# Optimization experiments

Measured on AMD Instinct MI355X. Metric: run time of the kernel, lower is better.

Reference implementation:

```python
import jax, jax.numpy as jnp
import numpy as np

N_NODES = 100000
TYPE_COUNTS = [40000, 40000, 20000]
RAW_DIMS = [512, 256, 128]
D = 64          # node_feature_dim
H = 8           # num_attention_heads
M = 2           # num_metapaths
E = 500000      # edges per metapath
SEM = 128       # semantic_attention_dim
NUM_CLS = 8
T = 40000       # num target nodes
SLOPE = 0.01    # leaky relu slope


def setup_inputs() -> dict:
    key = jax.random.key(0)
    ks = jax.random.split(key, 16)
    inp = {}
    inp['target_nodes'] = jax.random.randint(ks[0], (T,), 0, N_NODES)
    inp['metapath_0'] = jax.random.randint(ks[1], (E, 2), 0, N_NODES)
    inp['metapath_1'] = jax.random.randint(ks[2], (E, 2), 0, N_NODES)
    # contiguous blocks per node type (type t occupies a contiguous index range)
    inp['node_type_mapping'] = jnp.concatenate(
        [jnp.full((c,), t, dtype=jnp.int32) for t, c in enumerate(TYPE_COUNTS)])
    for t, (c, r) in enumerate(zip(TYPE_COUNTS, RAW_DIMS)):
        inp[f'node_feat_{t}'] = jax.random.normal(ks[3 + t], (c, r), dtype=jnp.float32)
        xav = float(np.sqrt(2.0) * np.sqrt(2.0 / (D + r)))
        inp[f'W{t}'] = jax.random.normal(ks[6 + t], (D, r), dtype=jnp.float32) * xav
        inp[f'b{t}'] = jnp.zeros((D,), dtype=jnp.float32)
    inp['node_attention'] = jax.random.normal(ks[9], (M, H, 2 * D), dtype=jnp.float32) * 0.05
    inp['Wsem'] = jax.random.normal(ks[10], (SEM, H * D), dtype=jnp.float32) * 0.05
    inp['bsem'] = jnp.zeros((SEM,), dtype=jnp.float32)
    inp['a_sem'] = jax.random.normal(ks[11], (SEM,), dtype=jnp.float32) * 0.05
    inp['Wcls'] = jax.random.normal(ks[12], (NUM_CLS, H * D), dtype=jnp.float32) * 0.05
    inp['bcls'] = jnp.zeros((NUM_CLS,), dtype=jnp.float32)
    return inp


def _metapath_agg(node_features, mp, attn_vec, target_nodes, n_nodes):
    # mp: [E, 2] (col 0 = neighbor/src, col -1 = current/dst); attn_vec: [H, 2D]
    src = mp[:, 0]
    dst = mp[:, -1]
    h_src = node_features[src]                        # [E, D] gather
    h_dst = node_features[dst]                        # [E, D] gather
    e = jnp.concatenate([h_dst, h_src], axis=-1)      # [E, 2D]
    score = e @ attn_vec.T                            # [E, H]
    score = jnp.where(score > 0, score, SLOPE * score)  # LeakyReLU
    # edge softmax over incoming edges of each destination node (per head)
    m = jax.ops.segment_max(score, dst, num_segments=n_nodes)
    ex = jnp.exp(score - m[dst])
    den = jax.ops.segment_sum(ex, dst, num_segments=n_nodes)
    attn = ex / den[dst]                              # [E, H]
    weighted = h_src[:, None, :] * attn[:, :, None]   # [E, H, D]
    agg = jax.ops.segment_sum(weighted, dst, num_segments=n_nodes)  # [N, H, D]
    return agg[target_nodes]                          # [T, H, D]


def reference(target_nodes, metapath_0, metapath_1, node_type_mapping,
              node_feat_0, node_feat_1, node_feat_2,
              W0, b0, W1, b1, W2, b2,
              node_attention, Wsem, bsem, a_sem, Wcls, bcls):
    n_nodes = node_type_mapping.shape[0]
    # node types are contiguous index blocks, so per-type projection + concat
    # reproduces the original scatter-by-type exactly (dropout rate is 0)
    node_features = jnp.concatenate([
        node_feat_0 @ W0.T + b0,
        node_feat_1 @ W1.T + b1,
        node_feat_2 @ W2.T + b2,
    ], axis=0)                                        # [N, D]
    h_list = [
        _metapath_agg(node_features, metapath_0, node_attention[0], target_nodes, n_nodes),
        _metapath_agg(node_features, metapath_1, node_attention[1], target_nodes, n_nodes),
    ]
    h = jnp.stack(h_list).reshape(M, -1, H * D)       # [M, T, H*D]
    s = jnp.tanh(jnp.einsum('mtd,sd->mts', h, Wsem) + bsem)  # [M, T, SEM]
    scores = jnp.mean(s @ a_sem, axis=1)              # [M] semantic attention
    beta = jax.nn.softmax(scores)                     # [M]
    embeddings = jnp.einsum('m,mtd->td', beta, h)     # [T, H*D]
    cls_logits = embeddings @ Wcls.T + bcls           # [T, NUM_CLS]
    return cls_logits, embeddings
```

## Files before the change

kernel.cpp:

```cpp
#include <hip/hip_runtime.h>
#include <hip/hip_bf16.h>

#define N_NODES 100000
#define EDGES   500000
#define T_TGT   40000
#define NH      8
#define NSEM    128
#define NCLS    8
#define SLOPE   0.01f
#define NCHUNK  25
#define PPAD    36

#define AS1 __attribute__((address_space(1)))
#define AS3 __attribute__((address_space(3)))

typedef __attribute__((ext_vector_type(8))) __bf16 bf16x8;
typedef __attribute__((ext_vector_type(4))) float f32x4;

__global__ __launch_bounds__(256) void proj_mfma(
        const float* __restrict__ A0, const float* __restrict__ W0,
        const float* __restrict__ b0,
        const float* __restrict__ A1, const float* __restrict__ W1,
        const float* __restrict__ b1,
        const float* __restrict__ A2, const float* __restrict__ W2,
        const float* __restrict__ b2,
        float* __restrict__ out) {
    __shared__ __bf16 Ah[2][128 * PPAD], Al[2][128 * PPAD];
    __shared__ __bf16 Wh[2][64 * PPAD],  Wl[2][64 * PPAD];
    int bx = blockIdx.x;
    const float *A, *W, *bias; int M, K, r0; float* op;
    if (bx < 313)      { A = A0; W = W0; bias = b0; M = 40000; K = 512;
                         r0 = bx * 128;         op = out; }
    else if (bx < 626) { A = A1; W = W1; bias = b1; M = 40000; K = 256;
                         r0 = (bx - 313) * 128; op = out + (size_t)40000 * 64; }
    else               { A = A2; W = W2; bias = b2; M = 20000; K = 128;
                         r0 = (bx - 626) * 128; op = out + (size_t)80000 * 64; }
    int tid = threadIdx.x;
    int wave = tid >> 6, lane = tid & 63;
    int arow = tid >> 1;
    int acol = (tid & 1) * 16;
    int wrow = tid & 63;
    int wcol = wave * 8;
    const float* Arp = A + (size_t)(r0 + arow) * K + acol;
    const float* Wrp = W + (size_t)wrow * K + wcol;
    bool aval = (r0 + arow) < M;

    float4 av0, av1, av2, av3, wv0, wv1;
    auto gload = [&](int k0) {
        float4 z = make_float4(0.f, 0.f, 0.f, 0.f);
        av0 = aval ? *(const float4*)(Arp + k0 + 0)  : z;
        av1 = aval ? *(const float4*)(Arp + k0 + 4)  : z;
        av2 = aval ? *(const float4*)(Arp + k0 + 8)  : z;
        av3 = aval ? *(const float4*)(Arp + k0 + 12) : z;
        wv0 = *(const float4*)(Wrp + k0 + 0);
        wv1 = *(const float4*)(Wrp + k0 + 4);
    };
    auto cvt_write = [&](int buf) {
        float xa[16] = {av0.x, av0.y, av0.z, av0.w, av1.x, av1.y, av1.z, av1.w,
                        av2.x, av2.y, av2.z, av2.w, av3.x, av3.y, av3.z, av3.w};
        bf16x8 ah2[2], al2[2];
        #pragma unroll
        for (int j = 0; j < 16; j++) {
            __bf16 h = (__bf16)xa[j];
            ah2[j >> 3][j & 7] = h;
            al2[j >> 3][j & 7] = (__bf16)(xa[j] - (float)h);
        }
        *(bf16x8*)&Ah[buf][arow * PPAD + acol]     = ah2[0];
        *(bf16x8*)&Ah[buf][arow * PPAD + acol + 8] = ah2[1];
        *(bf16x8*)&Al[buf][arow * PPAD + acol]     = al2[0];
        *(bf16x8*)&Al[buf][arow * PPAD + acol + 8] = al2[1];
        float xw[8] = {wv0.x, wv0.y, wv0.z, wv0.w, wv1.x, wv1.y, wv1.z, wv1.w};
        bf16x8 wh2, wl2;
        #pragma unroll
        for (int j = 0; j < 8; j++) {
            __bf16 h = (__bf16)xw[j];
            wh2[j] = h;
            wl2[j] = (__bf16)(xw[j] - (float)h);
        }
        *(bf16x8*)&Wh[buf][wrow * PPAD + wcol] = wh2;
        *(bf16x8*)&Wl[buf][wrow * PPAD + wcol] = wl2;
    };

    int mrow = lane & 15, koff = (lane >> 4) * 8;
    f32x4 acc[2][4] = {};
    int nsteps = K >> 5;

    gload(0);
    cvt_write(0);
    __syncthreads();
    for (int t = 0; t < nsteps; t++) {
        int cur = t & 1;
        if (t + 1 < nsteps) gload((t + 1) * 32);
        __builtin_amdgcn_sched_barrier(0);
        bf16x8 afh[2], afl[2], bfh[4], bfl[4];
        #pragma unroll
        for (int mi = 0; mi < 2; mi++) {
            int r = wave * 32 + mi * 16 + mrow;
            afh[mi] = *(const bf16x8*)&Ah[cur][r * PPAD + koff];
            afl[mi] = *(const bf16x8*)&Al[cur][r * PPAD + koff];
        }
        #pragma unroll
        for (int ni = 0; ni < 4; ni++) {
            int r = ni * 16 + mrow;
            bfh[ni] = *(const bf16x8*)&Wh[cur][r * PPAD + koff];
            bfl[ni] = *(const bf16x8*)&Wl[cur][r * PPAD + koff];
        }
        #pragma unroll
        for (int mi = 0; mi < 2; mi++)
            #pragma unroll
            for (int ni = 0; ni < 4; ni++) {
                acc[mi][ni] = __builtin_amdgcn_mfma_f32_16x16x32_bf16(afh[mi], bfh[ni], acc[mi][ni], 0, 0, 0);
                acc[mi][ni] = __builtin_amdgcn_mfma_f32_16x16x32_bf16(afh[mi], bfl[ni], acc[mi][ni], 0, 0, 0);
                acc[mi][ni] = __builtin_amdgcn_mfma_f32_16x16x32_bf16(afl[mi], bfh[ni], acc[mi][ni], 0, 0, 0);
            }
        if (t + 1 < nsteps) cvt_write(cur ^ 1);
        __syncthreads();
    }
    #pragma unroll
    for (int ni = 0; ni < 4; ni++) {
        int col = ni * 16 + mrow;
        float bv = bias[col];
        #pragma unroll
        for (int mi = 0; mi < 2; mi++) {
            int row = r0 + wave * 32 + mi * 16 + (lane >> 4) * 4;
            #pragma unroll
            for (int j = 0; j < 4; j++)
                if (row + j < M)
                    op[(size_t)(row + j) * 64 + col] = acc[mi][ni][j] + bv;
        }
    }
}

__global__ __launch_bounds__(256) void attn_proj(const float* __restrict__ nf,
        const float* __restrict__ na, float* __restrict__ proj) {
    __shared__ float ft[64][65];
    __shared__ float at[32][65];
    int tid = threadIdx.x;
    int n0 = blockIdx.x * 64;
    #pragma unroll
    for (int i = 0; i < 8; i++) {
        int lin = tid + i * 256;
        int j = lin >> 6, d = lin & 63;
        int m = j >> 4, side = (j >> 3) & 1, h = j & 7;
        at[j][d] = na[m * 1024 + h * 128 + side * 64 + d];
    }
    #pragma unroll
    for (int i = 0; i < 4; i++) {
        int lin = tid + i * 256;
        int row = lin >> 4;
        int c4 = (lin & 15) * 4;
        int gn = n0 + row;
        float4 v = make_float4(0.f, 0.f, 0.f, 0.f);
        if (gn < N_NODES) v = *(const float4*)(nf + (size_t)gn * 64 + c4);
        ft[row][c4 + 0] = v.x; ft[row][c4 + 1] = v.y;
        ft[row][c4 + 2] = v.z; ft[row][c4 + 3] = v.w;
    }
    __syncthreads();
    int node = tid >> 2;
    int jg = tid & 3;
    float acc[8] = {};
    for (int d = 0; d < 64; d++) {
        float f = ft[node][d];
        #pragma unroll
        for (int jj = 0; jj < 8; jj++)
            acc[jj] = fmaf(f, at[jg * 8 + jj][d], acc[jj]);
    }
    int gn = n0 + node;
    if (gn < N_NODES) {
        float4 o0 = make_float4(acc[0], acc[1], acc[2], acc[3]);
        float4 o1 = make_float4(acc[4], acc[5], acc[6], acc[7]);
        *(float4*)(proj + (size_t)gn * 32 + jg * 8) = o0;
        *(float4*)(proj + (size_t)gn * 32 + jg * 8 + 4) = o1;
    }
}

__global__ void hist_targets(const int* __restrict__ tgt, int* __restrict__ tcnt) {
    int i = blockIdx.x * 256 + threadIdx.x;
    if (i < T_TGT) atomicAdd(&tcnt[tgt[i]], 1);
}

__global__ void hist_edges(const int* __restrict__ mp, const int* __restrict__ tcnt,
                           int* __restrict__ ecnt) {
    int e = blockIdx.x * 256 + threadIdx.x;
    if (e < EDGES) {
        int dst = mp[2 * e + 1];
        if (tcnt[dst] > 0) atomicAdd(&ecnt[dst], 1);
    }
}

__global__ __launch_bounds__(1024) void scan_partial(const int* __restrict__ counts,
        int* __restrict__ partials) {
    int a = blockIdx.y, bx = blockIdx.x;
    const int* in = counts + (size_t)a * N_NODES;
    int base = bx * 4096 + threadIdx.x * 4;
    int s = 0;
    #pragma unroll
    for (int i = 0; i < 4; i++) {
        int idx = base + i;
        if (idx < N_NODES) s += in[idx];
    }
    #pragma unroll
    for (int off = 32; off; off >>= 1) s += __shfl_xor(s, off);
    __shared__ int red[16];
    int lane = threadIdx.x & 63, w = threadIdx.x >> 6;
    if (lane == 0) red[w] = s;
    __syncthreads();
    if (threadIdx.x < 16) {
        int x = red[threadIdx.x];
        #pragma unroll
        for (int off = 8; off; off >>= 1) x += __shfl_xor(x, off);
        if (threadIdx.x == 0) partials[a * 32 + bx] = x;
    }
}

__global__ void scan_partials(const int* __restrict__ partials,
        int* __restrict__ choff, int* __restrict__ offs) {
    int w = threadIdx.x >> 6, lane = threadIdx.x & 63;
    if (w < 3 && lane < 32) {
        int v = (lane < NCHUNK) ? partials[w * 32 + lane] : 0;
        int x = v;
        #pragma unroll
        for (int off = 1; off < 32; off <<= 1) {
            int y = __shfl_up(x, off);
            if (lane >= off) x += y;
        }
        if (lane < NCHUNK) choff[w * 32 + lane] = x - v;
        if (lane == NCHUNK - 1) offs[(size_t)w * (N_NODES + 1) + N_NODES] = x;
    }
}

__global__ __launch_bounds__(1024) void scan_final(const int* __restrict__ counts,
        const int* __restrict__ choff, int* __restrict__ offs, int* __restrict__ curs) {
    int a = blockIdx.y, bx = blockIdx.x;
    const int* in = counts + (size_t)a * N_NODES;
    int* out = offs + (size_t)a * (N_NODES + 1);
    int* cur = curs + (size_t)a * N_NODES;
    int tid = threadIdx.x, lane = tid & 63, w = tid >> 6;
    int base = bx * 4096 + tid * 4;
    int v[4], sum4 = 0;
    #pragma unroll
    for (int i = 0; i < 4; i++) {
        int idx = base + i;
        v[i] = (idx < N_NODES) ? in[idx] : 0;
        sum4 += v[i];
    }
    int x = sum4;
    #pragma unroll
    for (int off = 1; off < 64; off <<= 1) {
        int y = __shfl_up(x, off);
        if (lane >= off) x += y;
    }
    __shared__ int wred[16], wexc[16];
    if (lane == 63) wred[w] = x;
    __syncthreads();
    if (tid < 16) {
        int s = wred[tid], xs = s;
        #pragma unroll
        for (int off = 1; off < 16; off <<= 1) {
            int y = __shfl_up(xs, off);
            if (tid >= off) xs += y;
        }
        wexc[tid] = xs - s;
    }
    __syncthreads();
    int off0 = choff[a * 32 + bx] + wexc[w] + (x - sum4);
    int run = 0;
    #pragma unroll
    for (int i = 0; i < 4; i++) {
        int idx = base + i;
        if (idx < N_NODES) { out[idx] = off0 + run; cur[idx] = off0 + run; }
        run += v[i];
    }
}

__global__ void scatter_targets(const int* __restrict__ tgt, int* __restrict__ tcur,
                                int* __restrict__ tlist) {
    int i = blockIdx.x * 256 + threadIdx.x;
    if (i < T_TGT) {
        int n = tgt[i];
        int p = atomicAdd(&tcur[n], 1);
        tlist[p] = i;
    }
}

__global__ __launch_bounds__(256) void scatter_score(const int* __restrict__ mp,
        const int* __restrict__ tcnt, int* __restrict__ ecur,
        int* __restrict__ elist, __bf16* __restrict__ exs,
        const float* __restrict__ proj, int m) {
    int e = blockIdx.x * 256 + threadIdx.x;
    if (e >= EDGES) return;
    int src = mp[2 * e], dst = mp[2 * e + 1];
    if (tcnt[dst] <= 0) return;
    int p = atomicAdd(&ecur[dst], 1);
    elist[p] = src;
    const float* adp = proj + (size_t)dst * 32 + m * 16;
    const float* asp = proj + (size_t)src * 32 + m * 16 + 8;
    float4 ad0 = *(const float4*)(adp), ad1 = *(const float4*)(adp + 4);
    float4 as0 = *(const float4*)(asp), as1 = *(const float4*)(asp + 4);
    float ads[8] = {ad0.x, ad0.y, ad0.z, ad0.w, ad1.x, ad1.y, ad1.z, ad1.w};
    float ass[8] = {as0.x, as0.y, as0.z, as0.w, as1.x, as1.y, as1.z, as1.w};
    bf16x8 exv;
    #pragma unroll
    for (int h = 0; h < 8; h++) {
        float sc = ads[h] + ass[h];
        sc = sc > 0.f ? sc : SLOPE * sc;
        exv[h] = (__bf16)__expf(sc);
    }
    *(bf16x8*)(exs + (size_t)p * 8) = exv;
}

__global__ void build_ulist(const int* __restrict__ tcnt, int* __restrict__ ulist,
                            int* __restrict__ ucount) {
    int n = blockIdx.x * 256 + threadIdx.x;
    if (n < N_NODES && tcnt[n] > 0) {
        int u = atomicAdd(ucount, 1);
        ulist[u] = n;
    }
}

__global__ void cvt_bf16(const float* __restrict__ in, __bf16* __restrict__ out, int n) {
    int i = blockIdx.x * 256 + threadIdx.x;
    if (i < n) out[i] = (__bf16)in[i];
}

__global__ __launch_bounds__(256) void agg_kernel(
        const int* __restrict__ ulist, const int* __restrict__ ctrl_i,
        const int* __restrict__ offs,
        const int* __restrict__ esrc,
        const __bf16* __restrict__ exs,
        const float* __restrict__ nf,
        const int* __restrict__ tlist,
        __bf16* hb0, __bf16* hb1) {
    int m = blockIdx.y;
    int wslot = blockIdx.x * 4 + (threadIdx.x >> 6);
    int lane = threadIdx.x & 63;
    int ucount = ctrl_i[0];
    if (wslot >= ucount) return;
    int node = __builtin_amdgcn_readfirstlane(ulist[wslot]);
    const int* eo = offs + (size_t)m * (N_NODES + 1);
    int e0 = eo[node], e1 = eo[node + 1];
    const int* srcs = esrc + (size_t)m * EDGES;
    const __bf16* exm = exs + (size_t)m * EDGES * 8;
    float acc[8] = {};
    float dacc[8] = {};
    for (int e = e0; e < e1; e++) {
        int s = srcs[e];
        bf16x8 pb = *(const bf16x8*)(exm + (size_t)e * 8);
        float v = nf[(size_t)s * 64 + lane];
        #pragma unroll
        for (int h = 0; h < 8; h++) {
            float pw = (float)pb[h];
            dacc[h] += pw;
            acc[h] = fmaf(pw, v, acc[h]);
        }
    }
    #pragma unroll
    for (int h = 0; h < 8; h++)
        acc[h] *= (dacc[h] > 0.f) ? 1.0f / dacc[h] : 0.f;
    const int* to = offs + (size_t)2 * (N_NODES + 1);
    int t0 = to[node], t1 = to[node + 1];
    __bf16* hb = (m == 0) ? hb0 : hb1;
    for (int ti = t0; ti < t1; ti++) {
        int t = tlist[ti];
        __bf16* dst = hb + (size_t)t * 512;
        #pragma unroll
        for (int h = 0; h < 8; h++) dst[h * 64 + lane] = (__bf16)acc[h];
    }
}

__global__ __launch_bounds__(256) void sem_mfma(
        const __bf16* __restrict__ hb,
        const __bf16* __restrict__ Wb,
        const float* __restrict__ bsem, const float* __restrict__ a_sem,
        float* __restrict__ scores) {
    __shared__ __bf16 As[2][64 * 64];
    __shared__ __bf16 Bs[2][128 * 64];
    int m = blockIdx.y;
    int tid = threadIdx.x;
    int wave = tid >> 6, lane = tid & 63;
    const __bf16* A0 = hb + (size_t)m * T_TGT * 512 + (size_t)blockIdx.x * 64 * 512;

    int srow = lane >> 3;
    int scol = (lane & 7) * 8;

    auto stage = [&](int buf, int k0) {
        #pragma unroll
        for (int j = 0; j < 2; j++) {
            int row = j * 32 + wave * 8 + srow;
            const __bf16* gp = A0 + (size_t)row * 512 + k0 + scol;
            __bf16* lp = &As[buf][(j * 32 + wave * 8) * 64];
            __builtin_amdgcn_global_load_lds((const AS1 void*)gp,
                                             (AS3 void*)lp, 16, 0, 0);
        }
        #pragma unroll
        for (int j = 0; j < 4; j++) {
            int row = j * 32 + wave * 8 + srow;
            const __bf16* gp = Wb + (size_t)row * 512 + k0 + scol;
            __bf16* lp = &Bs[buf][(j * 32 + wave * 8) * 64];
            __builtin_amdgcn_global_load_lds((const AS1 void*)gp,
                                             (AS3 void*)lp, 16, 0, 0);
        }
    };

    int mrow = lane & 15;
    int kq = lane >> 4;
    f32x4 acc[4][2] = {};

    stage(0, 0);
    __syncthreads();
    for (int t = 0; t < 8; t++) {
        int cur = t & 1;
        if (t < 7) stage(cur ^ 1, (t + 1) * 64);
        __builtin_amdgcn_sched_barrier(0);
        const __bf16* Ab = &As[cur][0];
        const __bf16* Bb = &Bs[cur][0];
        #pragma unroll
        for (int kk = 0; kk < 2; kk++) {
            int ko = kk * 32 + kq * 8;
            bf16x8 a[4], b[2];
            #pragma unroll
            for (int r = 0; r < 4; r++)
                a[r] = *(const bf16x8*)(Ab + (r * 16 + mrow) * 64 + ko);
            #pragma unroll
            for (int c = 0; c < 2; c++)
                b[c] = *(const bf16x8*)(Bb + (wave * 32 + c * 16 + mrow) * 64 + ko);
            #pragma unroll
            for (int r = 0; r < 4; r++)
                #pragma unroll
                for (int c = 0; c < 2; c++)
                    acc[r][c] = __builtin_amdgcn_mfma_f32_16x16x32_bf16(a[r], b[c], acc[r][c], 0, 0, 0);
        }
        __syncthreads();
    }

    int n0 = wave * 32;
    float tot = 0.f;
    #pragma unroll
    for (int c = 0; c < 2; c++) {
        int col = n0 + c * 16 + (lane & 15);
        float bs = bsem[col], as = a_sem[col];
        #pragma unroll
        for (int r = 0; r < 4; r++)
            #pragma unroll
            for (int j = 0; j < 4; j++) {
                float x = acc[r][c][j] + bs;
                float th = 1.f - 2.f / (__expf(2.f * x) + 1.f);
                tot += th * as;
            }
    }
    __shared__ float red[256];
    red[threadIdx.x] = tot;
    __syncthreads();
    for (int s = 128; s; s >>= 1) {
        if (threadIdx.x < s) red[threadIdx.x] += red[threadIdx.x + s];
        __syncthreads();
    }
    if (threadIdx.x == 0) atomicAdd(&scores[m], red[0]);
}

__global__ void beta_kernel(const float* __restrict__ scores, float* __restrict__ beta) {
    if (threadIdx.x == 0) {
        float s0 = scores[0] / (float)T_TGT;
        float s1 = scores[1] / (float)T_TGT;
        float mx = fmaxf(s0, s1);
        float e0 = __expf(s0 - mx), e1 = __expf(s1 - mx);
        float inv = 1.f / (e0 + e1);
        beta[0] = e0 * inv;
        beta[1] = e1 * inv;
    }
}

__global__ __launch_bounds__(256) void emb_cls(
        const __bf16* __restrict__ hb0, const __bf16* __restrict__ hb1,
        const float* __restrict__ beta, const float* __restrict__ Wcls,
        const float* __restrict__ bcls, float* out_cls, float* out_emb) {
    __shared__ float Wl[8 * 512];
    int tid = threadIdx.x;
    #pragma unroll
    for (int i = 0; i < 16; i++) Wl[tid + i * 256] = Wcls[tid + i * 256];
    __syncthreads();
    int t = blockIdx.x * 4 + (tid >> 6);
    int lane = tid & 63;
    float b0 = beta[0], b1 = beta[1];
    bf16x8 v0 = *(const bf16x8*)(hb0 + (size_t)t * 512 + lane * 8);
    bf16x8 v1 = *(const bf16x8*)(hb1 + (size_t)t * 512 + lane * 8);
    float e[8];
    #pragma unroll
    for (int j = 0; j < 8; j++) e[j] = b0 * (float)v0[j] + b1 * (float)v1[j];
    float* ep = out_emb + (size_t)t * 512 + lane * 8;
    *(float4*)(ep + 0) = make_float4(e[0], e[1], e[2], e[3]);
    *(float4*)(ep + 4) = make_float4(e[4], e[5], e[6], e[7]);
    float pc[8];
    #pragma unroll
    for (int c = 0; c < 8; c++) {
        float4 w0 = *(const float4*)(Wl + c * 512 + lane * 8);
        float4 w1 = *(const float4*)(Wl + c * 512 + lane * 8 + 4);
        pc[c] = e[0] * w0.x + e[1] * w0.y + e[2] * w0.z + e[3] * w0.w
              + e[4] * w1.x + e[5] * w1.y + e[6] * w1.z + e[7] * w1.w;
    }
    #pragma unroll
    for (int off = 32; off; off >>= 1)
        #pragma unroll
        for (int c = 0; c < 8; c++) pc[c] += __shfl_xor(pc[c], off);
    if (lane == 0) {
        #pragma unroll
        for (int c = 0; c < 8; c++) out_cls[(size_t)t * 8 + c] = pc[c] + bcls[c];
    }
}

extern "C" void kernel_launch(void* const* d_in, const int* in_sizes, int n_in,
                              void* d_out, int out_size, void* d_ws, size_t ws_size,
                              hipStream_t stream) {
    const int* target = (const int*)d_in[0];
    const int* mp0 = (const int*)d_in[1];
    const int* mp1 = (const int*)d_in[2];
    const float* feat0 = (const float*)d_in[4];
    const float* W0 = (const float*)d_in[5];
    const float* b0 = (const float*)d_in[6];
    const float* feat1 = (const float*)d_in[7];
    const float* W1 = (const float*)d_in[8];
    const float* b1 = (const float*)d_in[9];
    const float* feat2 = (const float*)d_in[10];
    const float* W2 = (const float*)d_in[11];
    const float* b2 = (const float*)d_in[12];
    const float* natt = (const float*)d_in[13];
    const float* Wsem = (const float*)d_in[14];
    const float* bsem = (const float*)d_in[15];
    const float* asem = (const float*)d_in[16];
    const float* Wcls = (const float*)d_in[17];
    const float* bcls = (const float*)d_in[18];

    char* ws = (char*)d_ws;
    size_t off = 0;
    auto alloc = [&](size_t bytes) -> void* {
        void* p = ws + off;
        off += (bytes + 31) & ~(size_t)31;
        return p;
    };
    float* nf    = (float*)alloc((size_t)N_NODES * 64 * 4);
    float* proj  = (float*)alloc((size_t)N_NODES * 32 * 4);
    int* counts3 = (int*)alloc((size_t)3 * N_NODES * 4);
    int* offs3   = (int*)alloc((size_t)3 * (N_NODES + 1) * 4);
    int* curs3   = (int*)alloc((size_t)3 * N_NODES * 4);
    int* tlist   = (int*)alloc((size_t)T_TGT * 4);
    int* ulist   = (int*)alloc((size_t)N_NODES * 4);
    int* esrc    = (int*)alloc((size_t)2 * EDGES * 4);
    __bf16* exs  = (__bf16*)alloc((size_t)2 * EDGES * 8 * 2);
    int* partials = (int*)alloc((size_t)3 * 32 * 4);
    int* choff    = (int*)alloc((size_t)3 * 32 * 4);
    int* ctrl    = (int*)alloc(64);
    __bf16* Wsem_b = (__bf16*)alloc((size_t)NSEM * 512 * 2);
    __bf16* hb   = (__bf16*)alloc((size_t)2 * T_TGT * 512 * 2);
    if (off > ws_size) return;

    float* out_cls = (float*)d_out;
    float* out_emb = out_cls + (size_t)T_TGT * NCLS;
    __bf16* hb0 = hb;
    __bf16* hb1 = hb + (size_t)T_TGT * 512;
    float* ctrl_f = (float*)ctrl;
    float* scores = ctrl_f + 1;
    float* beta = ctrl_f + 3;

    hipMemsetAsync(counts3, 0, (size_t)3 * N_NODES * 4, stream);
    hipMemsetAsync(ctrl, 0, 64, stream);

    proj_mfma<<<dim3(783), 256, 0, stream>>>(feat0, W0, b0, feat1, W1, b1,
                                             feat2, W2, b2, nf);
    attn_proj<<<dim3(1563), 256, 0, stream>>>(nf, natt, proj);
    cvt_bf16<<<dim3(256), 256, 0, stream>>>(Wsem, Wsem_b, NSEM * 512);

    hist_targets<<<dim3(157), 256, 0, stream>>>(target, counts3 + 2 * N_NODES);
    hist_edges<<<dim3(1954), 256, 0, stream>>>(mp0, counts3 + 2 * N_NODES, counts3);
    hist_edges<<<dim3(1954), 256, 0, stream>>>(mp1, counts3 + 2 * N_NODES, counts3 + N_NODES);
    scan_partial<<<dim3(NCHUNK, 3), 1024, 0, stream>>>(counts3, partials);
    scan_partials<<<dim3(1), 192, 0, stream>>>(partials, choff, offs3);
    scan_final<<<dim3(NCHUNK, 3), 1024, 0, stream>>>(counts3, choff, offs3, curs3);
    scatter_targets<<<dim3(157), 256, 0, stream>>>(target, curs3 + 2 * N_NODES, tlist);
    scatter_score<<<dim3(1954), 256, 0, stream>>>(mp0, counts3 + 2 * N_NODES, curs3,
                                                  esrc, exs, proj, 0);
    scatter_score<<<dim3(1954), 256, 0, stream>>>(mp1, counts3 + 2 * N_NODES, curs3 + N_NODES,
                                                  esrc + EDGES, exs + (size_t)EDGES * 8, proj, 1);
    build_ulist<<<dim3(391), 256, 0, stream>>>(counts3 + 2 * N_NODES, ulist, ctrl);

    agg_kernel<<<dim3(10000, 2), 256, 0, stream>>>(ulist, ctrl, offs3, esrc, exs,
                                                   nf, tlist, hb0, hb1);
    sem_mfma<<<dim3(625, 2), 256, 0, stream>>>(hb, Wsem_b, bsem, asem, scores);
    beta_kernel<<<dim3(1), 64, 0, stream>>>(scores, beta);
    emb_cls<<<dim3(10000), 256, 0, stream>>>(hb0, hb1, beta, Wcls, bcls, out_cls, out_emb);
}
```

Measured before the change: 524.3 us.

## Stage projection tiles via direct global-to-LDS loads and pre-split weights

Weights are split into bf16 high/low parts once by a new small kernel. The projection GEMM then stages fp32 activation tiles and the pre-split weight tiles straight into LDS with global_load_lds, using an XOR-swizzled layout instead of padding. The hi/lo split of activations moves to the register path after the LDS read. The aim is to take register staging and conversion off the load path and to fetch and convert the weights only once. In exchange the conversion work in the MMA loop grows, LDS traffic for activations doubles because fp32 is stored, and one extra kernel launch is added.

```diff
diff --git a/kernel.cpp b/kernel.cpp
--- a/kernel.cpp
+++ b/kernel.cpp
@@ -9,7 +9,6 @@
 #define NCLS    8
 #define SLOPE   0.01f
 #define NCHUNK  25
-#define PPAD    36
 
 #define AS1 __attribute__((address_space(1)))
 #define AS3 __attribute__((address_space(3)))
@@ -17,103 +16,106 @@
 typedef __attribute__((ext_vector_type(8))) __bf16 bf16x8;
 typedef __attribute__((ext_vector_type(4))) float f32x4;
 
+__global__ void cvt_whl(const float* __restrict__ W0, const float* __restrict__ W1,
+                        const float* __restrict__ W2,
+                        __bf16* __restrict__ wh, __bf16* __restrict__ wl) {
+    int i = blockIdx.x * 256 + threadIdx.x;
+    float v;
+    if (i < 32768) v = W0[i];
+    else if (i < 49152) v = W1[i - 32768];
+    else if (i < 57344) v = W2[i - 49152];
+    else return;
+    __bf16 h = (__bf16)v;
+    wh[i] = h;
+    wl[i] = (__bf16)(v - (float)h);
+}
+
 __global__ __launch_bounds__(256) void proj_mfma(
-        const float* __restrict__ A0, const float* __restrict__ W0,
-        const float* __restrict__ b0,
-        const float* __restrict__ A1, const float* __restrict__ W1,
-        const float* __restrict__ b1,
-        const float* __restrict__ A2, const float* __restrict__ W2,
-        const float* __restrict__ b2,
+        const float* __restrict__ A0, const float* __restrict__ b0,
+        const float* __restrict__ A1, const float* __restrict__ b1,
+        const float* __restrict__ A2, const float* __restrict__ b2,
+        const __bf16* __restrict__ whb, const __bf16* __restrict__ wlb,
         float* __restrict__ out) {
-    __shared__ __bf16 Ah[2][128 * PPAD], Al[2][128 * PPAD];
-    __shared__ __bf16 Wh[2][64 * PPAD],  Wl[2][64 * PPAD];
+    __shared__ float  Asb[2][128 * 32];
+    __shared__ __bf16 Whs[2][64 * 32];
+    __shared__ __bf16 Wls[2][64 * 32];
     int bx = blockIdx.x;
-    const float *A, *W, *bias; int M, K, r0; float* op;
-    if (bx < 313)      { A = A0; W = W0; bias = b0; M = 40000; K = 512;
+    const float *A, *bias; int M, K, r0, woff; float* op;
+    if (bx < 313)      { A = A0; bias = b0; M = 40000; K = 512; woff = 0;
                          r0 = bx * 128;         op = out; }
-    else if (bx < 626) { A = A1; W = W1; bias = b1; M = 40000; K = 256;
+    else if (bx < 626) { A = A1; bias = b1; M = 40000; K = 256; woff = 32768;
                          r0 = (bx - 313) * 128; op = out + (size_t)40000 * 64; }
-    else               { A = A2; W = W2; bias = b2; M = 20000; K = 128;
+    else               { A = A2; bias = b2; M = 20000; K = 128; woff = 49152;
                          r0 = (bx - 626) * 128; op = out + (size_t)80000 * 64; }
+    const __bf16* Whp = whb + woff;
+    const __bf16* Wlp = wlb + woff;
     int tid = threadIdx.x;
     int wave = tid >> 6, lane = tid & 63;
-    int arow = tid >> 1;
-    int acol = (tid & 1) * 16;
-    int wrow = tid & 63;
-    int wcol = wave * 8;
-    const float* Arp = A + (size_t)(r0 + arow) * K + acol;
-    const float* Wrp = W + (size_t)wrow * K + wcol;
-    bool aval = (r0 + arow) < M;
-
-    float4 av0, av1, av2, av3, wv0, wv1;
-    auto gload = [&](int k0) {
-        float4 z = make_float4(0.f, 0.f, 0.f, 0.f);
-        av0 = aval ? *(const float4*)(Arp + k0 + 0)  : z;
-        av1 = aval ? *(const float4*)(Arp + k0 + 4)  : z;
-        av2 = aval ? *(const float4*)(Arp + k0 + 8)  : z;
-        av3 = aval ? *(const float4*)(Arp + k0 + 12) : z;
-        wv0 = *(const float4*)(Wrp + k0 + 0);
-        wv1 = *(const float4*)(Wrp + k0 + 4);
+
+    auto stage = [&](int buf, int k0) {
+        #pragma unroll
+        for (int j = 0; j < 4; j++) {
+            int rl = j * 32 + wave * 8 + (lane >> 3);
+            int g = r0 + rl; if (g > M - 1) g = M - 1;
+            int col = k0 + (((lane & 7) * 4) ^ ((rl & 3) << 3));
+            const float* gp = A + (size_t)g * K + col;
+            float* lp = &Asb[buf][(j * 32 + wave * 8) * 32];
+            __builtin_amdgcn_global_load_lds((const AS1 void*)gp,
+                                             (AS3 void*)lp, 16, 0, 0);
+        }
+        {
+            int rl = wave * 16 + (lane >> 2);
+            int col = k0 + (((lane & 3) * 8) ^ ((rl & 3) << 3));
+            const __bf16* gph = Whp + (size_t)rl * K + col;
+            __builtin_amdgcn_global_load_lds((const AS1 void*)gph,
+                    (AS3 void*)&Whs[buf][(wave * 16) * 32], 16, 0, 0);
+            const __bf16* gpl = Wlp + (size_t)rl * K + col;
+            __builtin_amdgcn_global_load_lds((const AS1 void*)gpl,
+                    (AS3 void*)&Wls[buf][(wave * 16) * 32], 16, 0, 0);
+        }
     };
-    auto cvt_write = [&](int buf) {
-        float xa[16] = {av0.x, av0.y, av0.z, av0.w, av1.x, av1.y, av1.z, av1.w,
-                        av2.x, av2.y, av2.z, av2.w, av3.x, av3.y, av3.z, av3.w};
-        bf16x8 ah2[2], al2[2];
-        #pragma unroll
-        for (int j = 0; j < 16; j++) {
-            __bf16 h = (__bf16)xa[j];
-            ah2[j >> 3][j & 7] = h;
-            al2[j >> 3][j & 7] = (__bf16)(xa[j] - (float)h);
-        }
-        *(bf16x8*)&Ah[buf][arow * PPAD + acol]     = ah2[0];
-        *(bf16x8*)&Ah[buf][arow * PPAD + acol + 8] = ah2[1];
-        *(bf16x8*)&Al[buf][arow * PPAD + acol]     = al2[0];
-        *(bf16x8*)&Al[buf][arow * PPAD + acol + 8] = al2[1];
-        float xw[8] = {wv0.x, wv0.y, wv0.z, wv0.w, wv1.x, wv1.y, wv1.z, wv1.w};
-        bf16x8 wh2, wl2;
-        #pragma unroll
-        for (int j = 0; j < 8; j++) {
-            __bf16 h = (__bf16)xw[j];
-            wh2[j] = h;
-            wl2[j] = (__bf16)(xw[j] - (float)h);
-        }
-        *(bf16x8*)&Wh[buf][wrow * PPAD + wcol] = wh2;
-        *(bf16x8*)&Wl[buf][wrow * PPAD + wcol] = wl2;
-    };
-
-    int mrow = lane & 15, koff = (lane >> 4) * 8;
+
+    int mrow = lane & 15, kq = lane >> 4;
     f32x4 acc[2][4] = {};
     int nsteps = K >> 5;
 
-    gload(0);
-    cvt_write(0);
+    stage(0, 0);
     __syncthreads();
     for (int t = 0; t < nsteps; t++) {
         int cur = t & 1;
-        if (t + 1 < nsteps) gload((t + 1) * 32);
+        if (t + 1 < nsteps) stage(cur ^ 1, (t + 1) * 32);
         __builtin_amdgcn_sched_barrier(0);
-        bf16x8 afh[2], afl[2], bfh[4], bfl[4];
+        bf16x8 ah[2], al[2], wh[4], wl[4];
         #pragma unroll
         for (int mi = 0; mi < 2; mi++) {
             int r = wave * 32 + mi * 16 + mrow;
-            afh[mi] = *(const bf16x8*)&Ah[cur][r * PPAD + koff];
-            afl[mi] = *(const bf16x8*)&Al[cur][r * PPAD + koff];
+            int off = (kq * 8) ^ ((r & 3) << 3);
+            const float* p = &Asb[cur][r * 32 + off];
+            f32x4 v0 = *(const f32x4*)p;
+            f32x4 v1 = *(const f32x4*)(p + 4);
+            #pragma unroll
+            for (int j = 0; j < 4; j++) {
+                __bf16 h0 = (__bf16)v0[j];
+                ah[mi][j] = h0; al[mi][j] = (__bf16)(v0[j] - (float)h0);
+                __bf16 h1 = (__bf16)v1[j];
+                ah[mi][j + 4] = h1; al[mi][j + 4] = (__bf16)(v1[j] - (float)h1);
+            }
         }
         #pragma unroll
         for (int ni = 0; ni < 4; ni++) {
             int r = ni * 16 + mrow;
-            bfh[ni] = *(const bf16x8*)&Wh[cur][r * PPAD + koff];
-            bfl[ni] = *(const bf16x8*)&Wl[cur][r * PPAD + koff];
+            int off = (kq * 8) ^ ((r & 3) << 3);
+            wh[ni] = *(const bf16x8*)&Whs[cur][r * 32 + off];
+            wl[ni] = *(const bf16x8*)&Wls[cur][r * 32 + off];
         }
         #pragma unroll
         for (int mi = 0; mi < 2; mi++)
             #pragma unroll
             for (int ni = 0; ni < 4; ni++) {
-                acc[mi][ni] = __builtin_amdgcn_mfma_f32_16x16x32_bf16(afh[mi], bfh[ni], acc[mi][ni], 0, 0, 0);
-                acc[mi][ni] = __builtin_amdgcn_mfma_f32_16x16x32_bf16(afh[mi], bfl[ni], acc[mi][ni], 0, 0, 0);
-                acc[mi][ni] = __builtin_amdgcn_mfma_f32_16x16x32_bf16(afl[mi], bfh[ni], acc[mi][ni], 0, 0, 0);
+                acc[mi][ni] = __builtin_amdgcn_mfma_f32_16x16x32_bf16(ah[mi], wh[ni], acc[mi][ni], 0, 0, 0);
+                acc[mi][ni] = __builtin_amdgcn_mfma_f32_16x16x32_bf16(ah[mi], wl[ni], acc[mi][ni], 0, 0, 0);
+                acc[mi][ni] = __builtin_amdgcn_mfma_f32_16x16x32_bf16(al[mi], wh[ni], acc[mi][ni], 0, 0, 0);
             }
-        if (t + 1 < nsteps) cvt_write(cur ^ 1);
         __syncthreads();
     }
     #pragma unroll
@@ -550,6 +552,8 @@
     int* choff    = (int*)alloc((size_t)3 * 32 * 4);
     int* ctrl    = (int*)alloc(64);
     __bf16* Wsem_b = (__bf16*)alloc((size_t)NSEM * 512 * 2);
+    __bf16* whb  = (__bf16*)alloc((size_t)57344 * 2);
+    __bf16* wlb  = (__bf16*)alloc((size_t)57344 * 2);
     __bf16* hb   = (__bf16*)alloc((size_t)2 * T_TGT * 512 * 2);
     if (off > ws_size) return;
 
@@ -564,8 +568,9 @@
     hipMemsetAsync(counts3, 0, (size_t)3 * N_NODES * 4, stream);
     hipMemsetAsync(ctrl, 0, 64, stream);
 
-    proj_mfma<<<dim3(783), 256, 0, stream>>>(feat0, W0, b0, feat1, W1, b1,
-                                             feat2, W2, b2, nf);
+    cvt_whl<<<dim3(224), 256, 0, stream>>>(W0, W1, W2, whb, wlb);
+    proj_mfma<<<dim3(783), 256, 0, stream>>>(feat0, b0, feat1, b1, feat2, b2,
+                                             whb, wlb, nf);
     attn_proj<<<dim3(1563), 256, 0, stream>>>(nf, natt, proj);
     cvt_bf16<<<dim3(256), 256, 0, stream>>>(Wsem, Wsem_b, NSEM * 512);
 
```

Result: faster. 476.9 us (-9.0%).
